# Performance work log

Hardware: AMD Instinct MI355X
Metric: run time of the kernel (lower is better)

Reference implementation:

```python
import jax, jax.numpy as jnp
import numpy as np

EPS = 1e-4  # LayerNorm epsilon from module


def layer_norm(x):
    # torch: (x - mean) / (std + eps), std unbiased (ddof=1), no affine
    mean = jnp.mean(x, axis=-1, keepdims=True)
    std = jnp.sqrt(jnp.var(x, axis=-1, ddof=1, keepdims=True))
    return (x - mean) / (std + EPS)


def setup_inputs() -> dict:
    key = jax.random.key(0)
    ks = jax.random.split(key, 9)
    B, S, D, H, QK = 2, 2048, 1024, 16, 64
    E = D // H  # per-head value/output dim
    scale = 0.02
    x = jax.random.normal(ks[0], (B, S, D), dtype=jnp.float32)
    # stacked per-head projection weights, Linear as x @ W + b
    Wq = jax.random.normal(ks[1], (H, D, QK), dtype=jnp.float32) * scale
    bq = jax.random.normal(ks[2], (H, QK), dtype=jnp.float32) * scale
    Wk = jax.random.normal(ks[3], (H, D, QK), dtype=jnp.float32) * scale
    bk = jax.random.normal(ks[4], (H, QK), dtype=jnp.float32) * scale
    Wv = jax.random.normal(ks[5], (H, D, E), dtype=jnp.float32) * scale
    bv = jax.random.normal(ks[6], (H, E), dtype=jnp.float32) * scale
    Wff = jax.random.normal(ks[7], (D, D), dtype=jnp.float32) * scale
    bff = jax.random.normal(ks[8], (D,), dtype=jnp.float32) * scale
    return {"x": x, "Wq": Wq, "bq": bq, "Wk": Wk, "bk": bk,
            "Wv": Wv, "bv": bv, "Wff": Wff, "bff": bff}


def reference(x, Wq, bq, Wk, bk, Wv, bv, Wff, bff):
    B, S, D = x.shape
    # all heads at once (vectorized over the Python per-head loop)
    Q = jnp.einsum('bsd,hdq->bhsq', x, Wq) + bq[None, :, None, :]
    K = jnp.einsum('bsd,hdq->bhsq', x, Wk) + bk[None, :, None, :]
    V = jnp.einsum('bsd,hde->bhse', x, Wv) + bv[None, :, None, :]
    scores = jnp.einsum('bhsq,bhtq->bhst', Q, K)  # [B,H,S,S]
    # masked_fill on tril(..., diagonal=-1): strictly-lower entries -> -inf
    mask = jnp.tril(jnp.ones((S, S), dtype=bool), k=-1)
    scores = jnp.where(mask[None, None], -jnp.inf, scores)
    # non-standard softmax axis: dim=-2 (over rows s, not keys t)
    attn = jax.nn.softmax(scores, axis=-2)
    heads = jnp.einsum('bhst,bhte->bhse', attn, V)  # [B,H,S,E]
    H, E = heads.shape[1], heads.shape[3]
    combined = heads.transpose(0, 2, 1, 3).reshape(B, S, H * E)  # concat heads
    x = layer_norm(x + combined)
    x = x + (x @ Wff + bff)
    return layer_norm(x)
```

## Files before the change

### kernel.cpp

```cpp
#include <hip/hip_runtime.h>
#include <hip/hip_bf16.h>
#include <math.h>

typedef unsigned short u16;
typedef unsigned int u32;
typedef __attribute__((ext_vector_type(8))) short short8;
typedef __attribute__((ext_vector_type(4))) short short4v;
typedef __attribute__((ext_vector_type(4))) float f32x4;

constexpr int B  = 2;
constexpr int S  = 2048;
constexpr int D  = 1024;
constexpr int H  = 16;
constexpr int DK = 64;
constexpr int BS = B * S;

__device__ __forceinline__ u16 f2b(float f) {
    __hip_bfloat16 h = __float2bfloat16(f);
    return *reinterpret_cast<u16*>(&h);
}
__device__ __forceinline__ float b2f(short s) {
    unsigned int u = ((unsigned int)(u16)s) << 16;
    return __builtin_bit_cast(float, u);
}

#define MFMA16(a, b, c) __builtin_amdgcn_mfma_f32_16x16x32_bf16((a), (b), (c), 0, 0, 0)

__device__ __forceinline__ void gload16(const u16* g, u16* l) {
    __builtin_amdgcn_global_load_lds(
        (const __attribute__((address_space(1))) u32*)g,
        (__attribute__((address_space(3))) u32*)l, 16, 0, 0);
}

__global__ __launch_bounds__(256) void convert_x(const float* __restrict__ src,
                                                 u16* __restrict__ dst)
{
    size_t i = ((size_t)blockIdx.x * 256 + threadIdx.x) * 8;
    f32x4 a = *reinterpret_cast<const f32x4*>(src + i);
    f32x4 b = *reinterpret_cast<const f32x4*>(src + i + 4);
    short8 o;
    o[0] = (short)f2b(a[0]); o[1] = (short)f2b(a[1]);
    o[2] = (short)f2b(a[2]); o[3] = (short)f2b(a[3]);
    o[4] = (short)f2b(b[0]); o[5] = (short)f2b(b[1]);
    o[6] = (short)f2b(b[2]); o[7] = (short)f2b(b[3]);
    *reinterpret_cast<short8*>(dst + i) = o;
}

__global__ __launch_bounds__(256) void tconv(const float* __restrict__ src,
                                             u16* __restrict__ dst, int R, int C)
{
    const int bb = blockIdx.z;
    src += (size_t)bb * R * C;
    dst += (size_t)bb * R * C;
    const int c0 = blockIdx.x * 64, r0 = blockIdx.y * 64;
    __shared__ float Ts[64][65];
    const int tid = threadIdx.x;
    #pragma unroll
    for (int i = 0; i < 4; ++i) {
        int idx = i * 1024 + tid * 4;
        int r = idx >> 6, c = idx & 63;
        f32x4 v = *reinterpret_cast<const f32x4*>(&src[(size_t)(r0 + r) * C + c0 + c]);
        Ts[r][c] = v[0]; Ts[r][c + 1] = v[1]; Ts[r][c + 2] = v[2]; Ts[r][c + 3] = v[3];
    }
    __syncthreads();
    #pragma unroll
    for (int i = 0; i < 4; ++i) {
        int cc = i * 16 + (tid >> 4);
        int rr = (tid & 15) * 4;
        short4v pk;
        pk[0] = (short)f2b(Ts[rr][cc]);     pk[1] = (short)f2b(Ts[rr + 1][cc]);
        pk[2] = (short)f2b(Ts[rr + 2][cc]); pk[3] = (short)f2b(Ts[rr + 3][cc]);
        *reinterpret_cast<short4v*>(&dst[(size_t)(c0 + cc) * R + r0 + rr]) = pk;
    }
}

__global__ __launch_bounds__(256) void qkv_gemm(
    const u16* __restrict__ xb, const u16* __restrict__ WT,
    const float* __restrict__ bq, const float* __restrict__ bk, const float* __restrict__ bv,
    u16* __restrict__ Qw, u16* __restrict__ Kw, u16* __restrict__ Vtw)
{
    const int id   = blockIdx.x;
    const int xcd  = id & 7;
    const int j    = id >> 3;
    const int nblk = xcd * 3 + j % 3;
    const int mblk = j / 3;
    const int m0 = mblk * 128, n0 = nblk * 128;
    const int sel = n0 >> 10;
    const float* bias = sel == 0 ? bq : sel == 1 ? bk : bv;

    __shared__ u16 SM[2][2][128][64];

    const int tid = threadIdx.x;
    const int w = tid >> 6, ln = tid & 15, hi = (tid & 63) >> 4;
    const int wm = w >> 1, wn = w & 1;
    const int l  = tid & 63;
    const int lr = l >> 3;
    const int lc8 = ((l & 7) ^ lr) * 8;

    char* sA0 = (char*)&SM[0][0][0][0];
    char* sB0 = (char*)&SM[0][1][0][0];
    char* sA1 = (char*)&SM[1][0][0][0];
    char* sB1 = (char*)&SM[1][1][0][0];
    auto swz = [](int r, int cb) { return r * 128 + (cb ^ ((r & 7) << 4)); };

    f32x4 acc[4][4];
    #pragma unroll
    for (int m = 0; m < 4; ++m)
        #pragma unroll
        for (int n = 0; n < 4; ++n) acc[m][n] = f32x4{0.f, 0.f, 0.f, 0.f};

    auto stage = [&](char* sa, char* sb, int k0) {
        #pragma unroll
        for (int c = 0; c < 4; ++c) {
            int rbase = w * 32 + c * 8;
            int row = rbase + lr;
            gload16(&xb[(size_t)(m0 + row) * D + k0 + lc8], (u16*)(sa + rbase * 128));
            gload16(&WT[(size_t)(n0 + row) * D + k0 + lc8], (u16*)(sb + rbase * 128));
        }
    };

    stage(sA0, sB0, 0);
    __syncthreads();

    for (int it = 0; it < 16; ++it) {
        char* ac = (it & 1) ? sA1 : sA0;
        char* bc = (it & 1) ? sB1 : sB0;
        if (it + 1 < 16)
            stage((it & 1) ? sA0 : sA1, (it & 1) ? sB0 : sB1, (it + 1) * 64);
        #pragma unroll
        for (int ks = 0; ks < 2; ++ks) {
            short8 af[4], bf[4];
            #pragma unroll
            for (int m = 0; m < 4; ++m)
                af[m] = *reinterpret_cast<const short8*>(
                    ac + swz(wm * 64 + m * 16 + ln, ks * 64 + hi * 16));
            #pragma unroll
            for (int n = 0; n < 4; ++n)
                bf[n] = *reinterpret_cast<const short8*>(
                    bc + swz(wn * 64 + n * 16 + ln, ks * 64 + hi * 16));
            #pragma unroll
            for (int m = 0; m < 4; ++m)
                #pragma unroll
                for (int n = 0; n < 4; ++n)
                    acc[m][n] = MFMA16(af[m], bf[n], acc[m][n]);
        }
        __syncthreads();
    }

    float bias4[4];
    #pragma unroll
    for (int n = 0; n < 4; ++n)
        bias4[n] = bias[(n0 & 1023) + wn * 64 + n * 16 + ln];

    char* eb = sA0;
    const int bidx  = m0 >> 11;
    const int sbase = m0 & 2047;
    const int h0    = (n0 & 1023) >> 6;

    if (sel < 2) {
        #pragma unroll
        for (int m = 0; m < 4; ++m)
            #pragma unroll
            for (int n = 0; n < 4; ++n)
                #pragma unroll
                for (int r = 0; r < 4; ++r) {
                    int row = wm * 64 + m * 16 + hi * 4 + r;
                    int col = wn * 64 + n * 16 + ln;
                    *reinterpret_cast<u16*>(eb + row * 256 + ((col * 2) ^ ((row & 7) << 4))) =
                        f2b(acc[m][n][r] + bias4[n]);
                }
        __syncthreads();
        u16* dst0 = sel == 0 ? Qw : Kw;
        #pragma unroll
        for (int c = 0; c < 8; ++c) {
            int idx = c * 256 + tid;
            int row = idx >> 4, g = idx & 15;
            short8 v = *reinterpret_cast<const short8*>(
                eb + row * 256 + ((g * 16) ^ ((row & 7) << 4)));
            int h = h0 + (g >> 3), j0 = (g & 7) * 8;
            *reinterpret_cast<short8*>(
                &dst0[((size_t)(bidx * H + h) * S + sbase + row) * DK + j0]) = v;
        }
    } else {
        #pragma unroll
        for (int m = 0; m < 4; ++m)
            #pragma unroll
            for (int n = 0; n < 4; ++n)
                #pragma unroll
                for (int r = 0; r < 4; ++r) {
                    int row = wm * 64 + m * 16 + hi * 4 + r;
                    int col = wn * 64 + n * 16 + ln;
                    *reinterpret_cast<u16*>(eb + col * 256 + ((row * 2) ^ ((col & 7) << 4))) =
                        f2b(acc[m][n][r] + bias4[n]);
                }
        __syncthreads();
        #pragma unroll
        for (int c = 0; c < 8; ++c) {
            int idx = c * 256 + tid;
            int e = idx >> 4, g = idx & 15;
            short8 v = *reinterpret_cast<const short8*>(
                eb + e * 256 + ((g * 16) ^ ((e & 7) << 4)));
            int h = h0 + (e >> 6), ein = e & 63;
            *reinterpret_cast<short8*>(
                &Vtw[((size_t)(bidx * H + h) * DK + ein) * S + sbase + g * 8]) = v;
        }
    }
}

__global__ __launch_bounds__(256) void col_stats(
    const u16* __restrict__ Qw, const u16* __restrict__ Kw,
    u16* __restrict__ Vtw)
{
    const int id = blockIdx.x;
    const int bh = (id & 7) * 4 + ((id >> 3) & 3);
    const int t0 = (31 - (id >> 5)) * 64;
    const u16* Qh = Qw + (size_t)bh * S * DK;
    const u16* Kh = Kw + (size_t)bh * S * DK;
    u16* Vh = Vtw + (size_t)bh * DK * S;

    __shared__ u16 Qs[2][64][64];
    __shared__ float zbuf[64];

    const int tid = threadIdx.x;
    const int w = tid >> 6, ln = tid & 15, hi = (tid & 63) >> 4;
    const int e0 = tid >> 3, sc = tid & 7;

    char* qb0 = (char*)&Qs[0][0][0];
    char* qb1 = (char*)&Qs[1][0][0];
    auto swz = [](int row, int colb) { return (row * 128 + colb) ^ ((row & 7) << 4); };

    short8 ak[2];
    #pragma unroll
    for (int ks = 0; ks < 2; ++ks)
        ak[ks] = *reinterpret_cast<const short8*>(
            &Kh[(size_t)(t0 + w * 16 + ln) * DK + ks * 32 + hi * 8]);

    float zs[4] = {0.f, 0.f, 0.f, 0.f};

    {
        short8 a = *reinterpret_cast<const short8*>(&Qh[(size_t)e0 * DK + sc * 8]);
        short8 b = *reinterpret_cast<const short8*>(&Qh[(size_t)(e0 + 32) * DK + sc * 8]);
        *reinterpret_cast<short8*>(qb0 + swz(e0, sc * 16)) = a;
        *reinterpret_cast<short8*>(qb0 + swz(e0 + 32, sc * 16)) = b;
    }
    __syncthreads();

    int cur = 0;
    for (int s0b = 0; s0b <= t0; s0b += 64) {
        const bool nxt = (s0b + 64 <= t0);
        short8 nq0, nq1;
        if (nxt) {
            nq0 = *reinterpret_cast<const short8*>(&Qh[(size_t)(s0b + 64 + e0) * DK + sc * 8]);
            nq1 = *reinterpret_cast<const short8*>(&Qh[(size_t)(s0b + 96 + e0) * DK + sc * 8]);
        }
        char* qb = cur ? qb1 : qb0;
        f32x4 c[4];
        #pragma unroll
        for (int n = 0; n < 4; ++n) c[n] = f32x4{0.f, 0.f, 0.f, 0.f};
        #pragma unroll
        for (int ks = 0; ks < 2; ++ks)
            #pragma unroll
            for (int n = 0; n < 4; ++n) {
                short8 bqf = *reinterpret_cast<const short8*>(
                    qb + swz(n * 16 + ln, ks * 64 + hi * 16));
                c[n] = MFMA16(ak[ks], bqf, c[n]);
            }
        if (s0b == t0) {
            #pragma unroll
            for (int n = 0; n < 4; ++n)
                #pragma unroll
                for (int r = 0; r < 4; ++r)
                    if (s0b + n * 16 + ln > t0 + w * 16 + hi * 4 + r)
                        c[n][r] = -INFINITY;
        }
        #pragma unroll
        for (int n = 0; n < 4; ++n)
            #pragma unroll
            for (int r = 0; r < 4; ++r)
                zs[r] += __expf(c[n][r]);
        if (nxt) {
            char* qn = cur ? qb0 : qb1;
            *reinterpret_cast<short8*>(qn + swz(e0, sc * 16)) = nq0;
            *reinterpret_cast<short8*>(qn + swz(e0 + 32, sc * 16)) = nq1;
        }
        __syncthreads();
        cur ^= 1;
    }

    #pragma unroll
    for (int r = 0; r < 4; ++r) {
        #pragma unroll
        for (int msk = 1; msk < 16; msk <<= 1)
            zs[r] += __shfl_xor(zs[r], msk, 64);
    }
    if (ln == 0) {
        #pragma unroll
        for (int r = 0; r < 4; ++r)
            zbuf[w * 16 + hi * 4 + r] = 1.f / zs[r];
    }
    __syncthreads();

    float iz[8];
    #pragma unroll
    for (int j = 0; j < 8; ++j) iz[j] = zbuf[sc * 8 + j];
    #pragma unroll
    for (int pass = 0; pass < 2; ++pass) {
        int e = e0 + 32 * pass;
        u16* vp = &Vh[(size_t)e * S + t0 + sc * 8];
        short8 v = *reinterpret_cast<short8*>(vp);
        short8 o;
        #pragma unroll
        for (int j = 0; j < 8; ++j) o[j] = (short)f2b(b2f(v[j]) * iz[j]);
        *reinterpret_cast<short8*>(vp) = o;
    }
}

__global__ __launch_bounds__(256) void attn_pv(
    const u16* __restrict__ Qw, const u16* __restrict__ Kw, const u16* __restrict__ Vtw,
    float* __restrict__ combined)
{
    const int id = blockIdx.x;
    const int bh = (id & 7) * 4 + ((id >> 3) & 3);
    const int s0 = (id >> 5) * 64;
    const int bidx = bh >> 4, h = bh & 15;
    const u16* Qh = Qw + (size_t)bh * S * DK;
    const u16* Kh = Kw + (size_t)bh * S * DK;
    const u16* Vh = Vtw + (size_t)bh * DK * S;

    __shared__ u16 Vs[2][64][64];
    __shared__ u16 Ps[64][72];

    const int tid = threadIdx.x;
    const int w = tid >> 6, ln = tid & 15, hi = (tid & 63) >> 4;
    const int e0 = tid >> 3, sc = tid & 7;

    char* vb0 = (char*)&Vs[0][0][0];
    char* vb1 = (char*)&Vs[1][0][0];
    auto swz = [](int row, int colb) { return (row * 128 + colb) ^ ((row & 7) << 4); };

    short8 bq[4][2];
    #pragma unroll
    for (int n = 0; n < 4; ++n)
        #pragma unroll
        for (int ks = 0; ks < 2; ++ks)
            bq[n][ks] = *reinterpret_cast<const short8*>(
                &Qh[(size_t)(s0 + n * 16 + ln) * DK + ks * 32 + hi * 8]);

    f32x4 acc[4];
    #pragma unroll
    for (int n = 0; n < 4; ++n) acc[n] = f32x4{0.f, 0.f, 0.f, 0.f};

    {
        short8 a = *reinterpret_cast<const short8*>(&Vh[(size_t)e0 * S + s0 + sc * 8]);
        short8 b = *reinterpret_cast<const short8*>(&Vh[(size_t)(e0 + 32) * S + s0 + sc * 8]);
        *reinterpret_cast<short8*>(vb0 + swz(e0, sc * 16)) = a;
        *reinterpret_cast<short8*>(vb0 + swz(e0 + 32, sc * 16)) = b;
    }

    short8 akA[2], akB[2];
    auto loadK = [&](short8 (&ak)[2], int t1) {
        #pragma unroll
        for (int ks = 0; ks < 2; ++ks)
            ak[ks] = *reinterpret_cast<const short8*>(
                &Kh[(size_t)(t1 + w * 16 + ln) * DK + ks * 32 + hi * 8]);
    };

    loadK(akA, s0);
    __syncthreads();
    int cur = 0;

    auto tile = [&](short8 (&ak)[2], int t1) {
        const bool nxt = (t1 + 64 < S);
        short8 nv0, nv1;
        if (nxt) {
            nv0 = *reinterpret_cast<const short8*>(&Vh[(size_t)e0 * S + t1 + 64 + sc * 8]);
            nv1 = *reinterpret_cast<const short8*>(&Vh[(size_t)(e0 + 32) * S + t1 + 64 + sc * 8]);
        }

        f32x4 st[4];
        #pragma unroll
        for (int n = 0; n < 4; ++n) st[n] = f32x4{0.f, 0.f, 0.f, 0.f};
        #pragma unroll
        for (int ks = 0; ks < 2; ++ks)
            #pragma unroll
            for (int n = 0; n < 4; ++n)
                st[n] = MFMA16(ak[ks], bq[n][ks], st[n]);

        const bool diag = (t1 == s0);
        #pragma unroll
        for (int n = 0; n < 4; ++n) {
            short4v pk;
            #pragma unroll
            for (int r = 0; r < 4; ++r) {
                float p = __expf(st[n][r]);
                if (diag && (s0 + n * 16 + ln) > (t1 + w * 16 + hi * 4 + r)) p = 0.f;
                pk[r] = (short)f2b(p);
            }
            *reinterpret_cast<short4v*>(&Ps[n * 16 + ln][w * 16 + hi * 4]) = pk;
        }
        __syncthreads();

        char* vb = cur ? vb1 : vb0;
        short8 pa[2];
        #pragma unroll
        for (int ks = 0; ks < 2; ++ks)
            pa[ks] = *reinterpret_cast<const short8*>(&Ps[w * 16 + ln][ks * 32 + hi * 8]);
        #pragma unroll
        for (int ks = 0; ks < 2; ++ks)
            #pragma unroll
            for (int n = 0; n < 4; ++n) {
                short8 vv = *reinterpret_cast<const short8*>(
                    vb + swz(n * 16 + ln, ks * 64 + hi * 16));
                acc[n] = MFMA16(pa[ks], vv, acc[n]);
            }

        if (nxt) {
            char* vn = cur ? vb0 : vb1;
            *reinterpret_cast<short8*>(vn + swz(e0, sc * 16)) = nv0;
            *reinterpret_cast<short8*>(vn + swz(e0 + 32, sc * 16)) = nv1;
        }
        __syncthreads();
        cur ^= 1;
    };

    int t1 = s0;
    while (t1 < S) {
        if (t1 + 64 < S) loadK(akB, t1 + 64);
        tile(akA, t1);
        t1 += 64;
        if (t1 >= S) break;
        if (t1 + 64 < S) loadK(akA, t1 + 64);
        tile(akB, t1);
        t1 += 64;
    }

    #pragma unroll
    for (int n = 0; n < 4; ++n)
        #pragma unroll
        for (int r = 0; r < 4; ++r) {
            int s = s0 + w * 16 + hi * 4 + r;
            combined[((size_t)bidx * S + s) * D + h * DK + n * 16 + ln] = acc[n][r];
        }
}

__global__ __launch_bounds__(256) void add_ln(
    const float* __restrict__ a, const float* __restrict__ bsrc,
    float* __restrict__ out, u16* __restrict__ outb)
{
    const int row = blockIdx.x;
    const int tid = threadIdx.x;
    const size_t base = (size_t)row * D;

    float v[4];
    float sum = 0.f;
    #pragma unroll
    for (int i = 0; i < 4; ++i) {
        int c = tid + i * 256;
        float t = a[base + c];
        if (bsrc) t += bsrc[base + c];
        v[i] = t;
        sum += t;
    }

    __shared__ float red[8];
    #pragma unroll
    for (int o = 32; o > 0; o >>= 1) sum += __shfl_down(sum, o, 64);
    const int lane = tid & 63, w = tid >> 6;
    if (lane == 0) red[w] = sum;
    __syncthreads();
    const float mean = (red[0] + red[1] + red[2] + red[3]) * (1.f / D);

    float s2 = 0.f;
    #pragma unroll
    for (int i = 0; i < 4; ++i) { float d2 = v[i] - mean; s2 += d2 * d2; }
    #pragma unroll
    for (int o = 32; o > 0; o >>= 1) s2 += __shfl_down(s2, o, 64);
    if (lane == 0) red[4 + w] = s2;
    __syncthreads();
    const float var = (red[4] + red[5] + red[6] + red[7]) * (1.f / (D - 1));
    const float scale = 1.f / (sqrtf(var) + 1e-4f);

    #pragma unroll
    for (int i = 0; i < 4; ++i) {
        int c = tid + i * 256;
        float o = (v[i] - mean) * scale;
        out[base + c] = o;
        if (outb) outb[base + c] = f2b(o);
    }
}

__global__ __launch_bounds__(256) void ffn(
    const float* __restrict__ x1, const u16* __restrict__ x1b,
    const u16* __restrict__ WffT, const float* __restrict__ bff,
    float* __restrict__ x2)
{
    const int id = blockIdx.x;
    const int m0 = ((id & 7) * 4 + ((id >> 3) & 3)) * 128;
    const int n0 = (id >> 5) * 128;

    __shared__ u16 SM[2][2][128][64];

    const int tid = threadIdx.x;
    const int w = tid >> 6, ln = tid & 15, hi = (tid & 63) >> 4;
    const int wm = w >> 1, wn = w & 1;
    const int l  = tid & 63;
    const int lr = l >> 3;
    const int lc8 = ((l & 7) ^ lr) * 8;

    char* sA0 = (char*)&SM[0][0][0][0];
    char* sB0 = (char*)&SM[0][1][0][0];
    char* sA1 = (char*)&SM[1][0][0][0];
    char* sB1 = (char*)&SM[1][1][0][0];
    auto swz = [](int r, int cb) { return r * 128 + (cb ^ ((r & 7) << 4)); };

    f32x4 acc[4][4];
    #pragma unroll
    for (int m = 0; m < 4; ++m)
        #pragma unroll
        for (int n = 0; n < 4; ++n) acc[m][n] = f32x4{0.f, 0.f, 0.f, 0.f};

    auto stage = [&](char* sa, char* sb, int k0) {
        #pragma unroll
        for (int c = 0; c < 4; ++c) {
            int rbase = w * 32 + c * 8;
            int row = rbase + lr;
            gload16(&x1b[(size_t)(m0 + row) * D + k0 + lc8], (u16*)(sa + rbase * 128));
            gload16(&WffT[(size_t)(n0 + row) * D + k0 + lc8], (u16*)(sb + rbase * 128));
        }
    };

    stage(sA0, sB0, 0);
    __syncthreads();

    for (int it = 0; it < 16; ++it) {
        char* ac = (it & 1) ? sA1 : sA0;
        char* bc = (it & 1) ? sB1 : sB0;
        if (it + 1 < 16)
            stage((it & 1) ? sA0 : sA1, (it & 1) ? sB0 : sB1, (it + 1) * 64);
        #pragma unroll
        for (int ks = 0; ks < 2; ++ks) {
            short8 af[4], bf[4];
            #pragma unroll
            for (int m = 0; m < 4; ++m)
                af[m] = *reinterpret_cast<const short8*>(
                    ac + swz(wm * 64 + m * 16 + ln, ks * 64 + hi * 16));
            #pragma unroll
            for (int n = 0; n < 4; ++n)
                bf[n] = *reinterpret_cast<const short8*>(
                    bc + swz(wn * 64 + n * 16 + ln, ks * 64 + hi * 16));
            #pragma unroll
            for (int m = 0; m < 4; ++m)
                #pragma unroll
                for (int n = 0; n < 4; ++n)
                    acc[m][n] = MFMA16(af[m], bf[n], acc[m][n]);
        }
        __syncthreads();
    }

    float bf4[4];
    #pragma unroll
    for (int n = 0; n < 4; ++n) bf4[n] = bff[n0 + wn * 64 + n * 16 + ln];

    #pragma unroll
    for (int m = 0; m < 4; ++m)
        #pragma unroll
        for (int n = 0; n < 4; ++n)
            #pragma unroll
            for (int r = 0; r < 4; ++r) {
                int row = m0 + wm * 64 + m * 16 + hi * 4 + r;
                int col = n0 + wn * 64 + n * 16 + ln;
                size_t idx = (size_t)row * D + col;
                x2[idx] = x1[idx] + acc[m][n][r] + bf4[n];
            }
}

extern "C" void kernel_launch(void* const* d_in, const int* in_sizes, int n_in,
                              void* d_out, int out_size, void* d_ws, size_t ws_size,
                              hipStream_t stream)
{
    const float* x   = (const float*)d_in[0];
    const float* Wq  = (const float*)d_in[1];
    const float* bq  = (const float*)d_in[2];
    const float* Wk  = (const float*)d_in[3];
    const float* bk  = (const float*)d_in[4];
    const float* Wv  = (const float*)d_in[5];
    const float* bv  = (const float*)d_in[6];
    const float* Wff = (const float*)d_in[7];
    const float* bff = (const float*)d_in[8];
    float* out = (float*)d_out;

    const size_t NX = (size_t)BS * D;
    char* p = (char*)d_ws;
    auto alloc = [&](size_t bytes) { char* r = p; p += bytes; return r; };

    u16* xb    = (u16*)alloc(NX * 2);
    u16* WT    = (u16*)alloc((size_t)3 * H * DK * D * 2);
    u16* WffT  = (u16*)alloc((size_t)D * D * 2);
    u16* Qw    = (u16*)alloc(NX * 2);
    u16* Kw    = (u16*)alloc(NX * 2);
    u16* Vtw   = (u16*)alloc(NX * 2);
    float* combined = (float*)alloc(NX * 4);
    float* x1       = (float*)alloc(NX * 4);
    u16*   x1b = xb;
    float* x2  = (float*)Qw;

    convert_x<<<dim3(NX / 2048), 256, 0, stream>>>(x, xb);
    tconv<<<dim3(1, 16, 16), 256, 0, stream>>>(Wq, WT, D, DK);
    tconv<<<dim3(1, 16, 16), 256, 0, stream>>>(Wk, WT + (size_t)H * DK * D, D, DK);
    tconv<<<dim3(1, 16, 16), 256, 0, stream>>>(Wv, WT + (size_t)2 * H * DK * D, D, DK);
    tconv<<<dim3(16, 16, 1), 256, 0, stream>>>(Wff, WffT, D, D);

    qkv_gemm<<<dim3(768), 256, 0, stream>>>(
        xb, WT, bq, bk, bv, Qw, Kw, Vtw);

    col_stats<<<dim3(1024), 256, 0, stream>>>(Qw, Kw, Vtw);

    attn_pv<<<dim3(1024), 256, 0, stream>>>(Qw, Kw, Vtw, combined);

    add_ln<<<BS, 256, 0, stream>>>(x, combined, x1, x1b);

    ffn<<<dim3(256), 256, 0, stream>>>(x1, x1b, WffT, bff, x2);

    add_ln<<<BS, 256, 0, stream>>>(x2, nullptr, out, nullptr);
}
```

Baseline: 151.7 us.

## Pair triangular tiles per block and software-pipeline QK with PV in attention

Both col_stats and attn_pv now launch half as many blocks. Each block handles two complementary 64-row tiles (pr and 31-pr), so every block does the same amount of causal-triangle work instead of some blocks getting long tails. attn_pv is also restructured: it double-buffers the P tile in shared memory and computes the next tile's scores and exponentials while doing the PV MFMAs for the current tile. This cuts the loop to one barrier per iteration instead of two. The trade-offs are fewer resident blocks, more shared memory per block and higher register pressure from holding the prefetched K and V fragments.

```diff
diff --git a/kernel.cpp b/kernel.cpp
--- a/kernel.cpp
+++ b/kernel.cpp
@@ -213,7 +213,7 @@
 {
     const int id = blockIdx.x;
     const int bh = (id & 7) * 4 + ((id >> 3) & 3);
-    const int t0 = (31 - (id >> 5)) * 64;
+    const int pr = id >> 5;
     const u16* Qh = Qw + (size_t)bh * S * DK;
     const u16* Kh = Kw + (size_t)bh * S * DK;
     u16* Vh = Vtw + (size_t)bh * DK * S;
@@ -229,90 +229,96 @@
     char* qb1 = (char*)&Qs[1][0][0];
     auto swz = [](int row, int colb) { return (row * 128 + colb) ^ ((row & 7) << 4); };
 
-    short8 ak[2];
-    #pragma unroll
-    for (int ks = 0; ks < 2; ++ks)
-        ak[ks] = *reinterpret_cast<const short8*>(
-            &Kh[(size_t)(t0 + w * 16 + ln) * DK + ks * 32 + hi * 8]);
-
-    float zs[4] = {0.f, 0.f, 0.f, 0.f};
-
-    {
-        short8 a = *reinterpret_cast<const short8*>(&Qh[(size_t)e0 * DK + sc * 8]);
-        short8 b = *reinterpret_cast<const short8*>(&Qh[(size_t)(e0 + 32) * DK + sc * 8]);
-        *reinterpret_cast<short8*>(qb0 + swz(e0, sc * 16)) = a;
-        *reinterpret_cast<short8*>(qb0 + swz(e0 + 32, sc * 16)) = b;
-    }
-    __syncthreads();
-
-    int cur = 0;
-    for (int s0b = 0; s0b <= t0; s0b += 64) {
-        const bool nxt = (s0b + 64 <= t0);
-        short8 nq0, nq1;
-        if (nxt) {
-            nq0 = *reinterpret_cast<const short8*>(&Qh[(size_t)(s0b + 64 + e0) * DK + sc * 8]);
-            nq1 = *reinterpret_cast<const short8*>(&Qh[(size_t)(s0b + 96 + e0) * DK + sc * 8]);
-        }
-        char* qb = cur ? qb1 : qb0;
-        f32x4 c[4];
-        #pragma unroll
-        for (int n = 0; n < 4; ++n) c[n] = f32x4{0.f, 0.f, 0.f, 0.f};
+    auto run_half = [&](int t0) {
+        short8 ak[2];
         #pragma unroll
         for (int ks = 0; ks < 2; ++ks)
-            #pragma unroll
-            for (int n = 0; n < 4; ++n) {
-                short8 bqf = *reinterpret_cast<const short8*>(
-                    qb + swz(n * 16 + ln, ks * 64 + hi * 16));
-                c[n] = MFMA16(ak[ks], bqf, c[n]);
-            }
-        if (s0b == t0) {
+            ak[ks] = *reinterpret_cast<const short8*>(
+                &Kh[(size_t)(t0 + w * 16 + ln) * DK + ks * 32 + hi * 8]);
+
+        float zs[4] = {0.f, 0.f, 0.f, 0.f};
+
+        {
+            short8 a = *reinterpret_cast<const short8*>(&Qh[(size_t)e0 * DK + sc * 8]);
+            short8 b = *reinterpret_cast<const short8*>(&Qh[(size_t)(e0 + 32) * DK + sc * 8]);
+            *reinterpret_cast<short8*>(qb0 + swz(e0, sc * 16)) = a;
+            *reinterpret_cast<short8*>(qb0 + swz(e0 + 32, sc * 16)) = b;
+        }
+        __syncthreads();
+
+        int cur = 0;
+        for (int s0b = 0; s0b <= t0; s0b += 64) {
+            const bool nxt = (s0b + 64 <= t0);
+            short8 nq0, nq1;
+            if (nxt) {
+                nq0 = *reinterpret_cast<const short8*>(&Qh[(size_t)(s0b + 64 + e0) * DK + sc * 8]);
+                nq1 = *reinterpret_cast<const short8*>(&Qh[(size_t)(s0b + 96 + e0) * DK + sc * 8]);
+            }
+            char* qb = cur ? qb1 : qb0;
+            f32x4 c[4];
+            #pragma unroll
+            for (int n = 0; n < 4; ++n) c[n] = f32x4{0.f, 0.f, 0.f, 0.f};
+            #pragma unroll
+            for (int ks = 0; ks < 2; ++ks)
+                #pragma unroll
+                for (int n = 0; n < 4; ++n) {
+                    short8 bqf = *reinterpret_cast<const short8*>(
+                        qb + swz(n * 16 + ln, ks * 64 + hi * 16));
+                    c[n] = MFMA16(ak[ks], bqf, c[n]);
+                }
+            if (s0b == t0) {
+                #pragma unroll
+                for (int n = 0; n < 4; ++n)
+                    #pragma unroll
+                    for (int r = 0; r < 4; ++r)
+                        if (s0b + n * 16 + ln > t0 + w * 16 + hi * 4 + r)
+                            c[n][r] = -INFINITY;
+            }
             #pragma unroll
             for (int n = 0; n < 4; ++n)
                 #pragma unroll
                 for (int r = 0; r < 4; ++r)
-                    if (s0b + n * 16 + ln > t0 + w * 16 + hi * 4 + r)
-                        c[n][r] = -INFINITY;
-        }
-        #pragma unroll
-        for (int n = 0; n < 4; ++n)
+                    zs[r] += __expf(c[n][r]);
+            if (nxt) {
+                char* qn = cur ? qb0 : qb1;
+                *reinterpret_cast<short8*>(qn + swz(e0, sc * 16)) = nq0;
+                *reinterpret_cast<short8*>(qn + swz(e0 + 32, sc * 16)) = nq1;
+            }
+            __syncthreads();
+            cur ^= 1;
+        }
+
+        #pragma unroll
+        for (int r = 0; r < 4; ++r) {
+            #pragma unroll
+            for (int msk = 1; msk < 16; msk <<= 1)
+                zs[r] += __shfl_xor(zs[r], msk, 64);
+        }
+        if (ln == 0) {
             #pragma unroll
             for (int r = 0; r < 4; ++r)
-                zs[r] += __expf(c[n][r]);
-        if (nxt) {
-            char* qn = cur ? qb0 : qb1;
-            *reinterpret_cast<short8*>(qn + swz(e0, sc * 16)) = nq0;
-            *reinterpret_cast<short8*>(qn + swz(e0 + 32, sc * 16)) = nq1;
-        }
-        __syncthreads();
-        cur ^= 1;
-    }
-
-    #pragma unroll
-    for (int r = 0; r < 4; ++r) {
-        #pragma unroll
-        for (int msk = 1; msk < 16; msk <<= 1)
-            zs[r] += __shfl_xor(zs[r], msk, 64);
-    }
-    if (ln == 0) {
-        #pragma unroll
-        for (int r = 0; r < 4; ++r)
-            zbuf[w * 16 + hi * 4 + r] = 1.f / zs[r];
-    }
-    __syncthreads();
-
-    float iz[8];
-    #pragma unroll
-    for (int j = 0; j < 8; ++j) iz[j] = zbuf[sc * 8 + j];
-    #pragma unroll
-    for (int pass = 0; pass < 2; ++pass) {
-        int e = e0 + 32 * pass;
-        u16* vp = &Vh[(size_t)e * S + t0 + sc * 8];
-        short8 v = *reinterpret_cast<short8*>(vp);
-        short8 o;
-        #pragma unroll
-        for (int j = 0; j < 8; ++j) o[j] = (short)f2b(b2f(v[j]) * iz[j]);
-        *reinterpret_cast<short8*>(vp) = o;
-    }
+                zbuf[w * 16 + hi * 4 + r] = 1.f / zs[r];
+        }
+        __syncthreads();
+
+        float iz[8];
+        #pragma unroll
+        for (int j = 0; j < 8; ++j) iz[j] = zbuf[sc * 8 + j];
+        #pragma unroll
+        for (int pass = 0; pass < 2; ++pass) {
+            int e = e0 + 32 * pass;
+            u16* vp = &Vh[(size_t)e * S + t0 + sc * 8];
+            short8 v = *reinterpret_cast<short8*>(vp);
+            short8 o;
+            #pragma unroll
+            for (int j = 0; j < 8; ++j) o[j] = (short)f2b(b2f(v[j]) * iz[j]);
+            *reinterpret_cast<short8*>(vp) = o;
+        }
+        __syncthreads();
+    };
+
+    run_half((31 - pr) * 64);
+    run_half(pr * 64);
 }
 
 __global__ __launch_bounds__(256) void attn_pv(
@@ -321,14 +327,15 @@
 {
     const int id = blockIdx.x;
     const int bh = (id & 7) * 4 + ((id >> 3) & 3);
-    const int s0 = (id >> 5) * 64;
+    const int pr = id >> 5;
     const int bidx = bh >> 4, h = bh & 15;
     const u16* Qh = Qw + (size_t)bh * S * DK;
     const u16* Kh = Kw + (size_t)bh * S * DK;
     const u16* Vh = Vtw + (size_t)bh * DK * S;
 
     __shared__ u16 Vs[2][64][64];
-    __shared__ u16 Ps[64][72];
+    __shared__ u16 Ps0a[64][72];
+    __shared__ u16 Ps1a[64][72];
 
     const int tid = threadIdx.x;
     const int w = tid >> 6, ln = tid & 15, hi = (tid & 63) >> 4;
@@ -338,109 +345,114 @@
     char* vb1 = (char*)&Vs[1][0][0];
     auto swz = [](int row, int colb) { return (row * 128 + colb) ^ ((row & 7) << 4); };
 
-    short8 bq[4][2];
-    #pragma unroll
-    for (int n = 0; n < 4; ++n)
-        #pragma unroll
-        for (int ks = 0; ks < 2; ++ks)
-            bq[n][ks] = *reinterpret_cast<const short8*>(
-                &Qh[(size_t)(s0 + n * 16 + ln) * DK + ks * 32 + hi * 8]);
-
-    f32x4 acc[4];
-    #pragma unroll
-    for (int n = 0; n < 4; ++n) acc[n] = f32x4{0.f, 0.f, 0.f, 0.f};
-
-    {
-        short8 a = *reinterpret_cast<const short8*>(&Vh[(size_t)e0 * S + s0 + sc * 8]);
-        short8 b = *reinterpret_cast<const short8*>(&Vh[(size_t)(e0 + 32) * S + s0 + sc * 8]);
-        *reinterpret_cast<short8*>(vb0 + swz(e0, sc * 16)) = a;
-        *reinterpret_cast<short8*>(vb0 + swz(e0 + 32, sc * 16)) = b;
-    }
-
-    short8 akA[2], akB[2];
-    auto loadK = [&](short8 (&ak)[2], int t1) {
-        #pragma unroll
-        for (int ks = 0; ks < 2; ++ks)
-            ak[ks] = *reinterpret_cast<const short8*>(
-                &Kh[(size_t)(t1 + w * 16 + ln) * DK + ks * 32 + hi * 8]);
+    auto run_half = [&](int s0) {
+        const int ntiles = (S - s0) >> 6;
+
+        short8 bq[4][2];
+        #pragma unroll
+        for (int n = 0; n < 4; ++n)
+            #pragma unroll
+            for (int ks = 0; ks < 2; ++ks)
+                bq[n][ks] = *reinterpret_cast<const short8*>(
+                    &Qh[(size_t)(s0 + n * 16 + ln) * DK + ks * 32 + hi * 8]);
+
+        f32x4 acc[4];
+        #pragma unroll
+        for (int n = 0; n < 4; ++n) acc[n] = f32x4{0.f, 0.f, 0.f, 0.f};
+
+        {
+            short8 nv0 = *reinterpret_cast<const short8*>(&Vh[(size_t)e0 * S + s0 + sc * 8]);
+            short8 nv1 = *reinterpret_cast<const short8*>(&Vh[(size_t)(e0 + 32) * S + s0 + sc * 8]);
+            short8 ak0 = *reinterpret_cast<const short8*>(&Kh[(size_t)(s0 + w * 16 + ln) * DK + hi * 8]);
+            short8 ak1 = *reinterpret_cast<const short8*>(&Kh[(size_t)(s0 + w * 16 + ln) * DK + 32 + hi * 8]);
+
+            *reinterpret_cast<short8*>(vb0 + swz(e0, sc * 16)) = nv0;
+            *reinterpret_cast<short8*>(vb0 + swz(e0 + 32, sc * 16)) = nv1;
+
+            f32x4 st[4];
+            #pragma unroll
+            for (int n = 0; n < 4; ++n) st[n] = f32x4{0.f, 0.f, 0.f, 0.f};
+            #pragma unroll
+            for (int n = 0; n < 4; ++n) {
+                st[n] = MFMA16(ak0, bq[n][0], st[n]);
+                st[n] = MFMA16(ak1, bq[n][1], st[n]);
+            }
+            #pragma unroll
+            for (int n = 0; n < 4; ++n) {
+                short4v pk;
+                #pragma unroll
+                for (int r = 0; r < 4; ++r) {
+                    float pv = __expf(st[n][r]);
+                    if ((n * 16 + ln) > (w * 16 + hi * 4 + r)) pv = 0.f;
+                    pk[r] = (short)f2b(pv);
+                }
+                *reinterpret_cast<short4v*>(&Ps0a[n * 16 + ln][w * 16 + hi * 4]) = pk;
+            }
+            __syncthreads();
+        }
+
+        for (int i = 0; i < ntiles; ++i) {
+            const int t1 = s0 + i * 64;
+            const bool nxt = (i + 1 < ntiles);
+            short8 nv0, nv1, ak0, ak1;
+            if (nxt) {
+                nv0 = *reinterpret_cast<const short8*>(&Vh[(size_t)e0 * S + t1 + 64 + sc * 8]);
+                nv1 = *reinterpret_cast<const short8*>(&Vh[(size_t)(e0 + 32) * S + t1 + 64 + sc * 8]);
+                ak0 = *reinterpret_cast<const short8*>(&Kh[(size_t)(t1 + 64 + w * 16 + ln) * DK + hi * 8]);
+                ak1 = *reinterpret_cast<const short8*>(&Kh[(size_t)(t1 + 64 + w * 16 + ln) * DK + 32 + hi * 8]);
+            }
+
+            {
+                const u16 (*Pc)[72] = (i & 1) ? Ps1a : Ps0a;
+                char* vc = (i & 1) ? vb1 : vb0;
+                short8 pa0 = *reinterpret_cast<const short8*>(&Pc[w * 16 + ln][hi * 8]);
+                short8 pa1 = *reinterpret_cast<const short8*>(&Pc[w * 16 + ln][32 + hi * 8]);
+                #pragma unroll
+                for (int n = 0; n < 4; ++n) {
+                    short8 vv0 = *reinterpret_cast<const short8*>(vc + swz(n * 16 + ln, hi * 16));
+                    short8 vv1 = *reinterpret_cast<const short8*>(vc + swz(n * 16 + ln, 64 + hi * 16));
+                    acc[n] = MFMA16(pa0, vv0, acc[n]);
+                    acc[n] = MFMA16(pa1, vv1, acc[n]);
+                }
+            }
+
+            if (nxt) {
+                f32x4 st[4];
+                #pragma unroll
+                for (int n = 0; n < 4; ++n) st[n] = f32x4{0.f, 0.f, 0.f, 0.f};
+                #pragma unroll
+                for (int n = 0; n < 4; ++n) {
+                    st[n] = MFMA16(ak0, bq[n][0], st[n]);
+                    st[n] = MFMA16(ak1, bq[n][1], st[n]);
+                }
+                u16 (*Pn)[72] = (i & 1) ? Ps0a : Ps1a;
+                #pragma unroll
+                for (int n = 0; n < 4; ++n) {
+                    short4v pk;
+                    #pragma unroll
+                    for (int r = 0; r < 4; ++r)
+                        pk[r] = (short)f2b(__expf(st[n][r]));
+                    *reinterpret_cast<short4v*>(&Pn[n * 16 + ln][w * 16 + hi * 4]) = pk;
+                }
+                char* vn = (i & 1) ? vb0 : vb1;
+                *reinterpret_cast<short8*>(vn + swz(e0, sc * 16)) = nv0;
+                *reinterpret_cast<short8*>(vn + swz(e0 + 32, sc * 16)) = nv1;
+                __syncthreads();
+            }
+        }
+
+        #pragma unroll
+        for (int n = 0; n < 4; ++n)
+            #pragma unroll
+            for (int r = 0; r < 4; ++r) {
+                int s = s0 + w * 16 + hi * 4 + r;
+                combined[((size_t)bidx * S + s) * D + h * DK + n * 16 + ln] = acc[n][r];
+            }
+        __syncthreads();
     };
 
-    loadK(akA, s0);
-    __syncthreads();
-    int cur = 0;
-
-    auto tile = [&](short8 (&ak)[2], int t1) {
-        const bool nxt = (t1 + 64 < S);
-        short8 nv0, nv1;
-        if (nxt) {
-            nv0 = *reinterpret_cast<const short8*>(&Vh[(size_t)e0 * S + t1 + 64 + sc * 8]);
-            nv1 = *reinterpret_cast<const short8*>(&Vh[(size_t)(e0 + 32) * S + t1 + 64 + sc * 8]);
-        }
-
-        f32x4 st[4];
-        #pragma unroll
-        for (int n = 0; n < 4; ++n) st[n] = f32x4{0.f, 0.f, 0.f, 0.f};
-        #pragma unroll
-        for (int ks = 0; ks < 2; ++ks)
-            #pragma unroll
-            for (int n = 0; n < 4; ++n)
-                st[n] = MFMA16(ak[ks], bq[n][ks], st[n]);
-
-        const bool diag = (t1 == s0);
-        #pragma unroll
-        for (int n = 0; n < 4; ++n) {
-            short4v pk;
-            #pragma unroll
-            for (int r = 0; r < 4; ++r) {
-                float p = __expf(st[n][r]);
-                if (diag && (s0 + n * 16 + ln) > (t1 + w * 16 + hi * 4 + r)) p = 0.f;
-                pk[r] = (short)f2b(p);
-            }
-            *reinterpret_cast<short4v*>(&Ps[n * 16 + ln][w * 16 + hi * 4]) = pk;
-        }
-        __syncthreads();
-
-        char* vb = cur ? vb1 : vb0;
-        short8 pa[2];
-        #pragma unroll
-        for (int ks = 0; ks < 2; ++ks)
-            pa[ks] = *reinterpret_cast<const short8*>(&Ps[w * 16 + ln][ks * 32 + hi * 8]);
-        #pragma unroll
-        for (int ks = 0; ks < 2; ++ks)
-            #pragma unroll
-            for (int n = 0; n < 4; ++n) {
-                short8 vv = *reinterpret_cast<const short8*>(
-                    vb + swz(n * 16 + ln, ks * 64 + hi * 16));
-                acc[n] = MFMA16(pa[ks], vv, acc[n]);
-            }
-
-        if (nxt) {
-            char* vn = cur ? vb0 : vb1;
-            *reinterpret_cast<short8*>(vn + swz(e0, sc * 16)) = nv0;
-            *reinterpret_cast<short8*>(vn + swz(e0 + 32, sc * 16)) = nv1;
-        }
-        __syncthreads();
-        cur ^= 1;
-    };
-
-    int t1 = s0;
-    while (t1 < S) {
-        if (t1 + 64 < S) loadK(akB, t1 + 64);
-        tile(akA, t1);
-        t1 += 64;
-        if (t1 >= S) break;
-        if (t1 + 64 < S) loadK(akA, t1 + 64);
-        tile(akB, t1);
-        t1 += 64;
-    }
-
-    #pragma unroll
-    for (int n = 0; n < 4; ++n)
-        #pragma unroll
-        for (int r = 0; r < 4; ++r) {
-            int s = s0 + w * 16 + hi * 4 + r;
-            combined[((size_t)bidx * S + s) * D + h * DK + n * 16 + ln] = acc[n][r];
-        }
+    run_half(pr * 64);
+    run_half((31 - pr) * 64);
 }
 
 __global__ __launch_bounds__(256) void add_ln(
@@ -613,9 +625,9 @@
     qkv_gemm<<<dim3(768), 256, 0, stream>>>(
         xb, WT, bq, bk, bv, Qw, Kw, Vtw);
 
-    col_stats<<<dim3(1024), 256, 0, stream>>>(Qw, Kw, Vtw);
-
-    attn_pv<<<dim3(1024), 256, 0, stream>>>(Qw, Kw, Vtw, combined);
+    col_stats<<<dim3(512), 256, 0, stream>>>(Qw, Kw, Vtw);
+
+    attn_pv<<<dim3(512), 256, 0, stream>>>(Qw, Kw, Vtw, combined);
 
     add_ln<<<BS, 256, 0, stream>>>(x, combined, x1, x1b);
 
```

Result: slower. 155.8 us (+2.7%).

## Split attention key range across two blocks per query tile and sum partials

Applied to the files above, without the earlier changes.

Each query tile's causal key range is split in half between two blocks, so the attention kernel launches twice as many blocks. This balances the triangular work, which previously gave some blocks up to 32 tiles and others only one. Each half writes its partial output to a separate fp32 buffer, and the following add+layernorm kernel sums both. In exchange it adds an extra fp32 buffer write and read, and the last tile's second-half block only writes zeros.

```diff
diff --git a/kernel.cpp b/kernel.cpp
--- a/kernel.cpp
+++ b/kernel.cpp
@@ -317,12 +317,36 @@
 
 __global__ __launch_bounds__(256) void attn_pv(
     const u16* __restrict__ Qw, const u16* __restrict__ Kw, const u16* __restrict__ Vtw,
-    float* __restrict__ combined)
+    float* __restrict__ O0, float* __restrict__ O1)
 {
     const int id = blockIdx.x;
     const int bh = (id & 7) * 4 + ((id >> 3) & 3);
-    const int s0 = (id >> 5) * 64;
+    const int j  = id >> 5;
+    const int p  = j >> 1;
+    const int half = j & 1;
+    const int s0 = p * 64;
+    const int ntot = 32 - p;
+    const int n0 = (ntot + 1) >> 1;
+    const int t_lo = half ? (p + n0) : p;
+    const int t_hi = half ? 32 : (p + n0);
     const int bidx = bh >> 4, h = bh & 15;
+    float* Opart = half ? O1 : O0;
+
+    const int tid = threadIdx.x;
+    const int w = tid >> 6, ln = tid & 15, hi = (tid & 63) >> 4;
+    const int e0 = tid >> 3, sc = tid & 7;
+
+    if (t_lo >= t_hi) {
+        #pragma unroll
+        for (int n = 0; n < 4; ++n)
+            #pragma unroll
+            for (int r = 0; r < 4; ++r) {
+                int s = s0 + w * 16 + hi * 4 + r;
+                Opart[((size_t)bidx * S + s) * D + h * DK + n * 16 + ln] = 0.f;
+            }
+        return;
+    }
+
     const u16* Qh = Qw + (size_t)bh * S * DK;
     const u16* Kh = Kw + (size_t)bh * S * DK;
     const u16* Vh = Vtw + (size_t)bh * DK * S;
@@ -330,10 +354,6 @@
     __shared__ u16 Vs[2][64][64];
     __shared__ u16 Ps[64][72];
 
-    const int tid = threadIdx.x;
-    const int w = tid >> 6, ln = tid & 15, hi = (tid & 63) >> 4;
-    const int e0 = tid >> 3, sc = tid & 7;
-
     char* vb0 = (char*)&Vs[0][0][0];
     char* vb1 = (char*)&Vs[1][0][0];
     auto swz = [](int row, int colb) { return (row * 128 + colb) ^ ((row & 7) << 4); };
@@ -350,9 +370,11 @@
     #pragma unroll
     for (int n = 0; n < 4; ++n) acc[n] = f32x4{0.f, 0.f, 0.f, 0.f};
 
+    const int tbeg = t_lo * 64, tend = t_hi * 64;
+
     {
-        short8 a = *reinterpret_cast<const short8*>(&Vh[(size_t)e0 * S + s0 + sc * 8]);
-        short8 b = *reinterpret_cast<const short8*>(&Vh[(size_t)(e0 + 32) * S + s0 + sc * 8]);
+        short8 a = *reinterpret_cast<const short8*>(&Vh[(size_t)e0 * S + tbeg + sc * 8]);
+        short8 b = *reinterpret_cast<const short8*>(&Vh[(size_t)(e0 + 32) * S + tbeg + sc * 8]);
         *reinterpret_cast<short8*>(vb0 + swz(e0, sc * 16)) = a;
         *reinterpret_cast<short8*>(vb0 + swz(e0 + 32, sc * 16)) = b;
     }
@@ -365,12 +387,12 @@
                 &Kh[(size_t)(t1 + w * 16 + ln) * DK + ks * 32 + hi * 8]);
     };
 
-    loadK(akA, s0);
+    loadK(akA, tbeg);
     __syncthreads();
     int cur = 0;
 
     auto tile = [&](short8 (&ak)[2], int t1) {
-        const bool nxt = (t1 + 64 < S);
+        const bool nxt = (t1 + 64 < tend);
         short8 nv0, nv1;
         if (nxt) {
             nv0 = *reinterpret_cast<const short8*>(&Vh[(size_t)e0 * S + t1 + 64 + sc * 8]);
@@ -392,9 +414,9 @@
             short4v pk;
             #pragma unroll
             for (int r = 0; r < 4; ++r) {
-                float p = __expf(st[n][r]);
-                if (diag && (s0 + n * 16 + ln) > (t1 + w * 16 + hi * 4 + r)) p = 0.f;
-                pk[r] = (short)f2b(p);
+                float pv = __expf(st[n][r]);
+                if (diag && (s0 + n * 16 + ln) > (t1 + w * 16 + hi * 4 + r)) pv = 0.f;
+                pk[r] = (short)f2b(pv);
             }
             *reinterpret_cast<short4v*>(&Ps[n * 16 + ln][w * 16 + hi * 4]) = pk;
         }
@@ -423,13 +445,13 @@
         cur ^= 1;
     };
 
-    int t1 = s0;
-    while (t1 < S) {
-        if (t1 + 64 < S) loadK(akB, t1 + 64);
+    int t1 = tbeg;
+    while (t1 < tend) {
+        if (t1 + 64 < tend) loadK(akB, t1 + 64);
         tile(akA, t1);
         t1 += 64;
-        if (t1 >= S) break;
-        if (t1 + 64 < S) loadK(akA, t1 + 64);
+        if (t1 >= tend) break;
+        if (t1 + 64 < tend) loadK(akA, t1 + 64);
         tile(akB, t1);
         t1 += 64;
     }
@@ -439,12 +461,13 @@
         #pragma unroll
         for (int r = 0; r < 4; ++r) {
             int s = s0 + w * 16 + hi * 4 + r;
-            combined[((size_t)bidx * S + s) * D + h * DK + n * 16 + ln] = acc[n][r];
-        }
-}
-
-__global__ __launch_bounds__(256) void add_ln(
-    const float* __restrict__ a, const float* __restrict__ bsrc,
+            Opart[((size_t)bidx * S + s) * D + h * DK + n * 16 + ln] = acc[n][r];
+        }
+}
+
+__global__ __launch_bounds__(256) void add_ln3(
+    const float* __restrict__ a, const float* __restrict__ o0,
+    const float* __restrict__ o1,
     float* __restrict__ out, u16* __restrict__ outb)
 {
     const int row = blockIdx.x;
@@ -456,8 +479,7 @@
     #pragma unroll
     for (int i = 0; i < 4; ++i) {
         int c = tid + i * 256;
-        float t = a[base + c];
-        if (bsrc) t += bsrc[base + c];
+        float t = a[base + c] + o0[base + c] + o1[base + c];
         v[i] = t;
         sum += t;
     }
@@ -485,7 +507,49 @@
         int c = tid + i * 256;
         float o = (v[i] - mean) * scale;
         out[base + c] = o;
-        if (outb) outb[base + c] = f2b(o);
+        outb[base + c] = f2b(o);
+    }
+}
+
+__global__ __launch_bounds__(256) void add_ln(
+    const float* __restrict__ a, float* __restrict__ out)
+{
+    const int row = blockIdx.x;
+    const int tid = threadIdx.x;
+    const size_t base = (size_t)row * D;
+
+    float v[4];
+    float sum = 0.f;
+    #pragma unroll
+    for (int i = 0; i < 4; ++i) {
+        int c = tid + i * 256;
+        float t = a[base + c];
+        v[i] = t;
+        sum += t;
+    }
+
+    __shared__ float red[8];
+    #pragma unroll
+    for (int o = 32; o > 0; o >>= 1) sum += __shfl_down(sum, o, 64);
+    const int lane = tid & 63, w = tid >> 6;
+    if (lane == 0) red[w] = sum;
+    __syncthreads();
+    const float mean = (red[0] + red[1] + red[2] + red[3]) * (1.f / D);
+
+    float s2 = 0.f;
+    #pragma unroll
+    for (int i = 0; i < 4; ++i) { float d2 = v[i] - mean; s2 += d2 * d2; }
+    #pragma unroll
+    for (int o = 32; o > 0; o >>= 1) s2 += __shfl_down(s2, o, 64);
+    if (lane == 0) red[4 + w] = s2;
+    __syncthreads();
+    const float var = (red[4] + red[5] + red[6] + red[7]) * (1.f / (D - 1));
+    const float scale = 1.f / (sqrtf(var) + 1e-4f);
+
+    #pragma unroll
+    for (int i = 0; i < 4; ++i) {
+        int c = tid + i * 256;
+        out[base + c] = (v[i] - mean) * scale;
     }
 }
 
@@ -599,8 +663,9 @@
     u16* Qw    = (u16*)alloc(NX * 2);
     u16* Kw    = (u16*)alloc(NX * 2);
     u16* Vtw   = (u16*)alloc(NX * 2);
-    float* combined = (float*)alloc(NX * 4);
-    float* x1       = (float*)alloc(NX * 4);
+    float* O0  = (float*)alloc(NX * 4);
+    float* O1  = (float*)alloc(NX * 4);
+    float* x1  = (float*)alloc(NX * 4);
     u16*   x1b = xb;
     float* x2  = (float*)Qw;
 
@@ -615,11 +680,11 @@
 
     col_stats<<<dim3(1024), 256, 0, stream>>>(Qw, Kw, Vtw);
 
-    attn_pv<<<dim3(1024), 256, 0, stream>>>(Qw, Kw, Vtw, combined);
-
-    add_ln<<<BS, 256, 0, stream>>>(x, combined, x1, x1b);
+    attn_pv<<<dim3(2048), 256, 0, stream>>>(Qw, Kw, Vtw, O0, O1);
+
+    add_ln3<<<BS, 256, 0, stream>>>(x, O0, O1, x1, x1b);
 
     ffn<<<dim3(256), 256, 0, stream>>>(x1, x1b, WffT, bff, x2);
 
-    add_ln<<<BS, 256, 0, stream>>>(x2, nullptr, out, nullptr);
-}
+    add_ln<<<BS, 256, 0, stream>>>(x2, out);
+}
```

Measured after the change: 158.8 us. +4.7%, slower.

## Stage Q/V tiles via async global_load_lds, use exp2 with prescaled Q, merge weight converts

Applied to the files above, without the earlier changes.

The Q and V double-buffer staging in col_stats and attn_pv now uses direct global-to-LDS loads instead of register loads followed by LDS stores. This removes register pressure and the store phase after the MFMAs. Q is prescaled by log2(e) in the QKV GEMM epilogue, so the softmax exponentials can use exp2 directly. The three per-weight transpose-convert launches are merged into one launch. The prescale is applied before bf16 rounding, which slightly changes numerics, and correctness relies on the async LDS writes being complete at the existing barriers.

```diff
diff --git a/kernel.cpp b/kernel.cpp
--- a/kernel.cpp
+++ b/kernel.cpp
@@ -14,6 +14,7 @@
 constexpr int H  = 16;
 constexpr int DK = 64;
 constexpr int BS = B * S;
+constexpr float LOG2E = 1.4426950408889634f;
 
 __device__ __forceinline__ u16 f2b(float f) {
     __hip_bfloat16 h = __float2bfloat16(f);
@@ -23,6 +24,7 @@
     unsigned int u = ((unsigned int)(u16)s) << 16;
     return __builtin_bit_cast(float, u);
 }
+__device__ __forceinline__ float fexp2(float x) { return __builtin_exp2f(x); }
 
 #define MFMA16(a, b, c) __builtin_amdgcn_mfma_f32_16x16x32_bf16((a), (b), (c), 0, 0, 0)
 
@@ -74,6 +76,37 @@
     }
 }
 
+__global__ __launch_bounds__(256) void tconv3(
+    const float* __restrict__ wq, const float* __restrict__ wk,
+    const float* __restrict__ wv, u16* __restrict__ dst)
+{
+    const int z = blockIdx.z;
+    const int selw = z >> 4, bb = z & 15;
+    const float* src = selw == 0 ? wq : selw == 1 ? wk : wv;
+    src += (size_t)bb * D * DK;
+    u16* d = dst + (size_t)selw * H * DK * D + (size_t)bb * D * DK;
+    const int r0 = blockIdx.y * 64;
+    __shared__ float Ts[64][65];
+    const int tid = threadIdx.x;
+    #pragma unroll
+    for (int i = 0; i < 4; ++i) {
+        int idx = i * 1024 + tid * 4;
+        int r = idx >> 6, c = idx & 63;
+        f32x4 v = *reinterpret_cast<const f32x4*>(&src[(size_t)(r0 + r) * DK + c]);
+        Ts[r][c] = v[0]; Ts[r][c + 1] = v[1]; Ts[r][c + 2] = v[2]; Ts[r][c + 3] = v[3];
+    }
+    __syncthreads();
+    #pragma unroll
+    for (int i = 0; i < 4; ++i) {
+        int cc = i * 16 + (tid >> 4);
+        int rr = (tid & 15) * 4;
+        short4v pk;
+        pk[0] = (short)f2b(Ts[rr][cc]);     pk[1] = (short)f2b(Ts[rr + 1][cc]);
+        pk[2] = (short)f2b(Ts[rr + 2][cc]); pk[3] = (short)f2b(Ts[rr + 3][cc]);
+        *reinterpret_cast<short4v*>(&d[(size_t)cc * D + r0 + rr]) = pk;
+    }
+}
+
 __global__ __launch_bounds__(256) void qkv_gemm(
     const u16* __restrict__ xb, const u16* __restrict__ WT,
     const float* __restrict__ bq, const float* __restrict__ bk, const float* __restrict__ bv,
@@ -87,6 +120,7 @@
     const int m0 = mblk * 128, n0 = nblk * 128;
     const int sel = n0 >> 10;
     const float* bias = sel == 0 ? bq : sel == 1 ? bk : bv;
+    const float qscale = (sel == 0) ? LOG2E : 1.0f;
 
     __shared__ u16 SM[2][2][128][64];
 
@@ -167,7 +201,7 @@
                     int row = wm * 64 + m * 16 + hi * 4 + r;
                     int col = wn * 64 + n * 16 + ln;
                     *reinterpret_cast<u16*>(eb + row * 256 + ((col * 2) ^ ((row & 7) << 4))) =
-                        f2b(acc[m][n][r] + bias4[n]);
+                        f2b((acc[m][n][r] + bias4[n]) * qscale);
                 }
         __syncthreads();
         u16* dst0 = sel == 0 ? Qw : Kw;
@@ -224,11 +258,21 @@
     const int tid = threadIdx.x;
     const int w = tid >> 6, ln = tid & 15, hi = (tid & 63) >> 4;
     const int e0 = tid >> 3, sc = tid & 7;
+    const int l = tid & 63, lr = l >> 3;
+    const int lc8 = ((l & 7) ^ lr) * 8;
 
     char* qb0 = (char*)&Qs[0][0][0];
     char* qb1 = (char*)&Qs[1][0][0];
     auto swz = [](int row, int colb) { return (row * 128 + colb) ^ ((row & 7) << 4); };
 
+    auto stageQ = [&](char* buf, int s) {
+        #pragma unroll
+        for (int c = 0; c < 2; ++c) {
+            int rbase = w * 16 + c * 8;
+            gload16(&Qh[(size_t)(s + rbase + lr) * DK + lc8], (u16*)(buf + rbase * 128));
+        }
+    };
+
     short8 ak[2];
     #pragma unroll
     for (int ks = 0; ks < 2; ++ks)
@@ -237,22 +281,12 @@
 
     float zs[4] = {0.f, 0.f, 0.f, 0.f};
 
-    {
-        short8 a = *reinterpret_cast<const short8*>(&Qh[(size_t)e0 * DK + sc * 8]);
-        short8 b = *reinterpret_cast<const short8*>(&Qh[(size_t)(e0 + 32) * DK + sc * 8]);
-        *reinterpret_cast<short8*>(qb0 + swz(e0, sc * 16)) = a;
-        *reinterpret_cast<short8*>(qb0 + swz(e0 + 32, sc * 16)) = b;
-    }
+    stageQ(qb0, 0);
     __syncthreads();
 
     int cur = 0;
     for (int s0b = 0; s0b <= t0; s0b += 64) {
-        const bool nxt = (s0b + 64 <= t0);
-        short8 nq0, nq1;
-        if (nxt) {
-            nq0 = *reinterpret_cast<const short8*>(&Qh[(size_t)(s0b + 64 + e0) * DK + sc * 8]);
-            nq1 = *reinterpret_cast<const short8*>(&Qh[(size_t)(s0b + 96 + e0) * DK + sc * 8]);
-        }
+        if (s0b + 64 <= t0) stageQ(cur ? qb0 : qb1, s0b + 64);
         char* qb = cur ? qb1 : qb0;
         f32x4 c[4];
         #pragma unroll
@@ -277,12 +311,7 @@
         for (int n = 0; n < 4; ++n)
             #pragma unroll
             for (int r = 0; r < 4; ++r)
-                zs[r] += __expf(c[n][r]);
-        if (nxt) {
-            char* qn = cur ? qb0 : qb1;
-            *reinterpret_cast<short8*>(qn + swz(e0, sc * 16)) = nq0;
-            *reinterpret_cast<short8*>(qn + swz(e0 + 32, sc * 16)) = nq1;
-        }
+                zs[r] += fexp2(c[n][r]);
         __syncthreads();
         cur ^= 1;
     }
@@ -332,12 +361,21 @@
 
     const int tid = threadIdx.x;
     const int w = tid >> 6, ln = tid & 15, hi = (tid & 63) >> 4;
-    const int e0 = tid >> 3, sc = tid & 7;
+    const int l = tid & 63, lr = l >> 3;
+    const int lc8 = ((l & 7) ^ lr) * 8;
 
     char* vb0 = (char*)&Vs[0][0][0];
     char* vb1 = (char*)&Vs[1][0][0];
     auto swz = [](int row, int colb) { return (row * 128 + colb) ^ ((row & 7) << 4); };
 
+    auto stageV = [&](char* buf, int t) {
+        #pragma unroll
+        for (int c = 0; c < 2; ++c) {
+            int rbase = w * 16 + c * 8;
+            gload16(&Vh[(size_t)(rbase + lr) * S + t + lc8], (u16*)(buf + rbase * 128));
+        }
+    };
+
     short8 bq[4][2];
     #pragma unroll
     for (int n = 0; n < 4; ++n)
@@ -349,13 +387,6 @@
     f32x4 acc[4];
     #pragma unroll
     for (int n = 0; n < 4; ++n) acc[n] = f32x4{0.f, 0.f, 0.f, 0.f};
-
-    {
-        short8 a = *reinterpret_cast<const short8*>(&Vh[(size_t)e0 * S + s0 + sc * 8]);
-        short8 b = *reinterpret_cast<const short8*>(&Vh[(size_t)(e0 + 32) * S + s0 + sc * 8]);
-        *reinterpret_cast<short8*>(vb0 + swz(e0, sc * 16)) = a;
-        *reinterpret_cast<short8*>(vb0 + swz(e0 + 32, sc * 16)) = b;
-    }
 
     short8 akA[2], akB[2];
     auto loadK = [&](short8 (&ak)[2], int t1) {
@@ -365,17 +396,14 @@
                 &Kh[(size_t)(t1 + w * 16 + ln) * DK + ks * 32 + hi * 8]);
     };
 
+    stageV(vb0, s0);
     loadK(akA, s0);
     __syncthreads();
     int cur = 0;
 
     auto tile = [&](short8 (&ak)[2], int t1) {
         const bool nxt = (t1 + 64 < S);
-        short8 nv0, nv1;
-        if (nxt) {
-            nv0 = *reinterpret_cast<const short8*>(&Vh[(size_t)e0 * S + t1 + 64 + sc * 8]);
-            nv1 = *reinterpret_cast<const short8*>(&Vh[(size_t)(e0 + 32) * S + t1 + 64 + sc * 8]);
-        }
+        if (nxt) stageV(cur ? vb0 : vb1, t1 + 64);
 
         f32x4 st[4];
         #pragma unroll
@@ -392,9 +420,9 @@
             short4v pk;
             #pragma unroll
             for (int r = 0; r < 4; ++r) {
-                float p = __expf(st[n][r]);
-                if (diag && (s0 + n * 16 + ln) > (t1 + w * 16 + hi * 4 + r)) p = 0.f;
-                pk[r] = (short)f2b(p);
+                float pv = fexp2(st[n][r]);
+                if (diag && (s0 + n * 16 + ln) > (t1 + w * 16 + hi * 4 + r)) pv = 0.f;
+                pk[r] = (short)f2b(pv);
             }
             *reinterpret_cast<short4v*>(&Ps[n * 16 + ln][w * 16 + hi * 4]) = pk;
         }
@@ -413,12 +441,6 @@
                     vb + swz(n * 16 + ln, ks * 64 + hi * 16));
                 acc[n] = MFMA16(pa[ks], vv, acc[n]);
             }
-
-        if (nxt) {
-            char* vn = cur ? vb0 : vb1;
-            *reinterpret_cast<short8*>(vn + swz(e0, sc * 16)) = nv0;
-            *reinterpret_cast<short8*>(vn + swz(e0 + 32, sc * 16)) = nv1;
-        }
         __syncthreads();
         cur ^= 1;
     };
@@ -605,9 +627,7 @@
     float* x2  = (float*)Qw;
 
     convert_x<<<dim3(NX / 2048), 256, 0, stream>>>(x, xb);
-    tconv<<<dim3(1, 16, 16), 256, 0, stream>>>(Wq, WT, D, DK);
-    tconv<<<dim3(1, 16, 16), 256, 0, stream>>>(Wk, WT + (size_t)H * DK * D, D, DK);
-    tconv<<<dim3(1, 16, 16), 256, 0, stream>>>(Wv, WT + (size_t)2 * H * DK * D, D, DK);
+    tconv3<<<dim3(1, 16, 48), 256, 0, stream>>>(Wq, Wk, Wv, WT);
     tconv<<<dim3(16, 16, 1), 256, 0, stream>>>(Wff, WffT, D, D);
 
     qkv_gemm<<<dim3(768), 256, 0, stream>>>(
```

Measured after the change: 154.4 us. Within noise of the previous version (+1.8%).
